# Performance work log

Hardware: AMD Instinct MI355X
Metric: run time of the kernel (lower is better)

## Reference

```python
import jax, jax.numpy as jnp
import numpy as np

ROPE_THETA = 10000.0


def apply_rope(q, k, cos, sin):
    # q,k: [B,H,S,D]; cos,sin: [S,D/2] -> broadcast [1,1,S,D/2]
    def rot(t):
        t2 = t.reshape(*t.shape[:-1], -1, 2)  # [B,H,S,D/2,2]
        te, to = t2[..., 0], t2[..., 1]
        c = cos[None, None, :, :]
        s = sin[None, None, :, :]
        re = te * c - to * s
        im = te * s + to * c
        return jnp.stack([re, im], axis=-1).reshape(t.shape)
    return rot(q), rot(k)


def setup_inputs() -> dict:
    key = jax.random.key(0)
    ks = jax.random.split(key, 4)
    B, S, D, H = 2, 2048, 1024, 16
    hd = D // H
    x = jax.random.normal(ks[0], (B, S, D), dtype=jnp.float32)
    # causal boolean mask (True = keep)
    mask = jnp.tril(jnp.ones((S, S), dtype=bool))[None, None]
    # rotary tables
    inv_freq = 1.0 / (ROPE_THETA ** (jnp.arange(0, hd, 2, dtype=jnp.float32) / hd))  # [hd/2]
    t = jnp.arange(S, dtype=jnp.float32)
    ang = t[:, None] * inv_freq[None, :]  # [S, hd/2]
    freqs_cos = jnp.cos(ang)
    freqs_sin = jnp.sin(ang)
    W_qkv = jax.random.normal(ks[1], (D, 3 * D), dtype=jnp.float32) * 0.02
    b_qkv = jnp.zeros((3 * D,), dtype=jnp.float32)
    W_o = jax.random.normal(ks[2], (D, D), dtype=jnp.float32) * 0.02
    b_o = jnp.zeros((D,), dtype=jnp.float32)
    return {"x": x, "mask": mask, "freqs_cos": freqs_cos, "freqs_sin": freqs_sin,
            "W_qkv": W_qkv, "b_qkv": b_qkv, "W_o": W_o, "b_o": b_o}


def reference(x, mask, freqs_cos, freqs_sin, W_qkv, b_qkv, W_o, b_o):
    B, S, D = x.shape
    H = 16
    hd = D // H
    scale = hd ** -0.5
    qkv = x @ W_qkv + b_qkv  # [B,S,3D]
    q, k, v = jnp.split(qkv, 3, axis=-1)
    q = q.reshape(B, S, H, hd).transpose(0, 2, 1, 3)  # [B,H,S,hd]
    k = k.reshape(B, S, H, hd).transpose(0, 2, 1, 3)
    v = v.reshape(B, S, H, hd).transpose(0, 2, 1, 3)
    q, k = apply_rope(q, k, freqs_cos, freqs_sin)
    scores = jnp.einsum('bhqd,bhkd->bhqk', q, k) * scale
    scores = jnp.where(mask, scores, jnp.finfo(scores.dtype).min)
    attn = jax.nn.softmax(scores, axis=-1)
    out = jnp.einsum('bhqk,bhkd->bhqd', attn, v)
    out = out.transpose(0, 2, 1, 3).reshape(B, S, D)
    return out @ W_o + b_o
```

## Files before the change

kernel.cpp:

```cpp
#include <hip/hip_runtime.h>
#include <hip/hip_bf16.h>
#include <stdint.h>

typedef unsigned short u16;
typedef __attribute__((ext_vector_type(8))) __bf16 bf16x8;
typedef __attribute__((ext_vector_type(4))) float f32x4;
typedef __attribute__((ext_vector_type(16))) float f32x16;
typedef __attribute__((ext_vector_type(8))) u16 u16x8;

__device__ __forceinline__ u16 f2bf(float f) {
  union { float f; unsigned int u; } v; v.f = f;
  unsigned int r = v.u + 0x7fffu + ((v.u >> 16) & 1u);
  return (u16)(r >> 16);
}
__device__ __forceinline__ unsigned pack2(float lo, float hi) {
  return (unsigned)f2bf(lo) | ((unsigned)f2bf(hi) << 16);
}

__device__ __forceinline__ f32x4 mfma16(bf16x8 a, bf16x8 b, f32x4 c) {
  return __builtin_amdgcn_mfma_f32_16x16x32_bf16(a, b, c, 0, 0, 0);
}
__device__ __forceinline__ f32x16 mfma32(bf16x8 a, bf16x8 b, f32x16 c) {
  return __builtin_amdgcn_mfma_f32_32x32x16_bf16(a, b, c, 0, 0, 0);
}

__device__ __forceinline__ void gload16(const void* g, void* l) {
  __builtin_amdgcn_global_load_lds((const __attribute__((address_space(1))) void*)g,
                                   (__attribute__((address_space(3))) void*)l,
                                   16, 0, 0);
}

__global__ void cast_bf16_kernel(const float* __restrict__ in, u16* __restrict__ out, int n) {
  int i = (blockIdx.x * 256 + threadIdx.x) * 8;
  if (i >= n) return;
  const float4* p = (const float4*)(in + i);
  float4 a = p[0], b = p[1];
  u16x8 o;
  o[0] = f2bf(a.x); o[1] = f2bf(a.y); o[2] = f2bf(a.z); o[3] = f2bf(a.w);
  o[4] = f2bf(b.x); o[5] = f2bf(b.y); o[6] = f2bf(b.z); o[7] = f2bf(b.w);
  *(u16x8*)(out + i) = o;
}

__global__ void transpose_cast_k(const float* __restrict__ in, u16* __restrict__ out,
                                 int R, int Ccols) {
  __shared__ float tile[64][65];
  const int c0 = (int)blockIdx.x << 6, r0 = (int)blockIdx.y << 6;
  const int tx = threadIdx.x & 63, ty = threadIdx.x >> 6;
#pragma unroll
  for (int i = ty; i < 64; i += 4)
    tile[i][tx] = in[(size_t)(r0 + i) * Ccols + c0 + tx];
  __syncthreads();
#pragma unroll
  for (int i = ty; i < 64; i += 4)
    out[(size_t)(c0 + i) * R + r0 + tx] = f2bf(tile[tx][i]);
}

__global__ __launch_bounds__(256, 2)
void gemm_qkv(const u16* __restrict__ A, const u16* __restrict__ Bt,
              const float* __restrict__ bias,
              const float* __restrict__ fc, const float* __restrict__ fs,
              u16* __restrict__ qr, u16* __restrict__ kr, u16* __restrict__ vr) {
  const int K = 1024;
  __shared__ __align__(16) u16 smem[128 * 136];
  u16* const As = smem;
  u16* const Bs = smem + 128 * 32;
  const int m0 = (int)(blockIdx.x / 24) << 7;
  const int n0 = (int)(blockIdx.x % 24) << 7;
  const int tid = threadIdx.x;
  const int l = tid & 63, lg = l >> 4, ll = l & 15;
  const int w = tid >> 6;
  const int wr = (w >> 1) << 6, wc = (w & 1) << 6;
  const int srow = tid >> 2, scol = (tid & 3) << 3;
  const u16* ga = A + (size_t)(m0 + srow) * K + scol;
  const u16* gb = Bt + (size_t)(n0 + srow) * K + scol;
  u16* la0 = &As[srow * 32 + scol];
  u16* la1 = &As[(srow + 64) * 32 + scol];
  u16* lb0 = &Bs[srow * 32 + scol];
  u16* lb1 = &Bs[(srow + 64) * 32 + scol];
  const size_t K64 = (size_t)64 * K;
  f32x4 acc[4][4] = {};
  for (int kt = 0; kt < K; kt += 32) {
    gload16(ga + kt, la0);
    gload16(ga + kt + K64, la1);
    gload16(gb + kt, lb0);
    gload16(gb + kt + K64, lb1);
    __syncthreads();
    bf16x8 a[4], b[4];
#pragma unroll
    for (int i = 0; i < 4; ++i) {
      a[i] = *(const bf16x8*)&As[(wr + i * 16 + ll) * 32 + lg * 8];
      b[i] = *(const bf16x8*)&Bs[(wc + i * 16 + ll) * 32 + lg * 8];
    }
#pragma unroll
    for (int mi = 0; mi < 4; ++mi)
#pragma unroll
      for (int ni = 0; ni < 4; ++ni)
        acc[mi][ni] = mfma16(a[mi], b[ni], acc[mi][ni]);
    __syncthreads();
  }
  const int sec = n0 >> 10;
  u16* const dst = (sec == 0) ? qr : (sec == 1) ? kr : vr;
  const int h0 = (n0 & 1023) >> 6;
#pragma unroll
  for (int ni = 0; ni < 4; ++ni) {
    const int cc = wc + ni * 16 + ll;
    const int n = n0 + cc;
    const int d = n & 63;
    const float bi_ = bias[n];
    const int i2 = d >> 1;
    const bool odd = d & 1;
#pragma unroll
    for (int mi = 0; mi < 4; ++mi) {
#pragma unroll
      for (int r = 0; r < 4; ++r) {
        const int rr = wr + mi * 16 + lg * 4 + r;
        const int s = (m0 + rr) & 2047;
        float v = acc[mi][ni][r] + bi_;
        if (sec < 2) {
          const float c = fc[s * 32 + i2], sn = fs[s * 32 + i2];
          const float p = __shfl_xor(v, 1);
          v = odd ? (p * sn + v * c) : (v * c - p * sn);
          if (sec == 0) v *= 0.125f;
        }
        smem[rr * 136 + cc] = f2bf(v);
      }
    }
  }
  __syncthreads();
#pragma unroll
  for (int it = 0; it < 8; ++it) {
    const int c = it * 256 + tid;
    const int j = c & 7, hh = (c >> 3) & 1, rr = c >> 4;
    const int row = m0 + rr;
    const int bb = row >> 11, ss = row & 2047;
    const uint4 val = *(const uint4*)&smem[rr * 136 + hh * 64 + j * 8];
    *(uint4*)&dst[((size_t)(((bb << 4) + h0 + hh) << 11) + ss) * 64 + j * 8] = val;
  }
}

__global__ __launch_bounds__(256, 2)
void gemm_bt(const u16* __restrict__ A, const u16* __restrict__ Bt,
             const float* __restrict__ bias, float* __restrict__ C,
             int M, int N, int K) {
  __shared__ u16 As[128 * 32];
  __shared__ u16 Bs[128 * 32];
  const int nb = N >> 7;
  const int m0 = (int)(blockIdx.x / nb) << 7;
  const int n0 = (int)(blockIdx.x % nb) << 7;
  const int tid = threadIdx.x;
  const int l = tid & 63, lg = l >> 4, ll = l & 15;
  const int w = tid >> 6;
  const int wr = (w >> 1) << 6, wc = (w & 1) << 6;
  const int srow = tid >> 2, scol = (tid & 3) << 3;
  const u16* ga = A + (size_t)(m0 + srow) * K + scol;
  const u16* gb = Bt + (size_t)(n0 + srow) * K + scol;
  u16* la0 = &As[srow * 32 + scol];
  u16* la1 = &As[(srow + 64) * 32 + scol];
  u16* lb0 = &Bs[srow * 32 + scol];
  u16* lb1 = &Bs[(srow + 64) * 32 + scol];
  const size_t K64 = (size_t)64 * K;
  f32x4 acc[4][4] = {};
  for (int kt = 0; kt < K; kt += 32) {
    gload16(ga + kt, la0);
    gload16(ga + kt + K64, la1);
    gload16(gb + kt, lb0);
    gload16(gb + kt + K64, lb1);
    __syncthreads();
    bf16x8 a[4], b[4];
#pragma unroll
    for (int i = 0; i < 4; ++i) {
      a[i] = *(const bf16x8*)&As[(wr + i * 16 + ll) * 32 + lg * 8];
      b[i] = *(const bf16x8*)&Bs[(wc + i * 16 + ll) * 32 + lg * 8];
    }
#pragma unroll
    for (int mi = 0; mi < 4; ++mi)
#pragma unroll
      for (int ni = 0; ni < 4; ++ni)
        acc[mi][ni] = mfma16(a[mi], b[ni], acc[mi][ni]);
    __syncthreads();
  }
#pragma unroll
  for (int mi = 0; mi < 4; ++mi) {
#pragma unroll
    for (int r = 0; r < 4; ++r) {
      const int row = m0 + wr + mi * 16 + lg * 4 + r;
      float* crow = C + (size_t)row * N + n0 + wc;
#pragma unroll
      for (int ni = 0; ni < 4; ++ni)
        crow[ni * 16 + ll] = acc[mi][ni][r] + bias[n0 + wc + ni * 16 + ll];
    }
  }
}

__global__ void v_transpose_bf16(const u16* __restrict__ vr, u16* __restrict__ vt) {
  __shared__ u16 tile[64][66];
  const int bh = blockIdx.x;
  const int s0 = (int)blockIdx.y << 6;
  const int tx = threadIdx.x & 63, ty = threadIdx.x >> 6;
#pragma unroll
  for (int i = ty; i < 64; i += 4)
    tile[i][tx] = vr[((size_t)bh * 2048 + s0 + i) * 64 + tx];
  __syncthreads();
#pragma unroll
  for (int i = ty; i < 64; i += 4)
    vt[((size_t)bh * 64 + i) * 2048 + s0 + tx] = tile[tx][i];
}

__global__ __launch_bounds__(256, 2)
void attn_k(const u16* __restrict__ qr, const u16* __restrict__ kr,
            const u16* __restrict__ vt, u16* __restrict__ aout) {
  __shared__ __align__(16) char kvlds[16384];
  const int bi = (int)blockIdx.x;
  const int bh = bi & 31;
  const int qt = (bi < 256) ? (15 - (bi >> 5)) : ((bi - 256) >> 5);
  const int tid = threadIdx.x;
  const int w = tid >> 6, l = tid & 63, hi = l >> 5, ql = l & 31;
  const u16* Q  = qr + (size_t)bh * (2048 * 64);
  const u16* Kp = kr + (size_t)bh * (2048 * 64);
  const u16* Vp = vt + (size_t)bh * (64 * 2048);
  const int q0w = (qt << 7) + (w << 5);
  const int qg = q0w + ql;
  bf16x8 qf[4];
#pragma unroll
  for (int mi = 0; mi < 4; ++mi)
    qf[mi] = *(const bf16x8*)&Q[(size_t)qg * 64 + mi * 16 + hi * 8];
  const int sr = tid >> 2, sc = (tid & 3) * 32;
  const int wo0 = (sr * 128 + sc) ^ ((sr & 7) << 4);
  const int wo1 = (sr * 128 + sc + 16) ^ ((sr & 7) << 4);
  const char* kga = (const char*)(Kp + (size_t)sr * 64) + sc;
  const char* vga = (const char*)(Vp + (size_t)sr * 2048) + sc;
  const int swz = (ql & 7) << 4;
  f32x16 oa = {}, ob = {};
  float mrow = -1e30f, lp = 0.f;
  const int nch = 2 * qt + 2;
  uint4 sk0 = *(const uint4*)(kga), sk1 = *(const uint4*)(kga + 16);
  uint4 sv0 = *(const uint4*)(vga), sv1 = *(const uint4*)(vga + 16);
  for (int ch = 0; ch < nch; ++ch) {
    asm volatile("s_waitcnt vmcnt(0)" ::: "memory");
    asm volatile("s_barrier" ::: "memory");
    *(uint4*)(kvlds + wo0) = sk0;
    *(uint4*)(kvlds + wo1) = sk1;
    *(uint4*)(kvlds + 8192 + wo0) = sv0;
    *(uint4*)(kvlds + 8192 + wo1) = sv1;
    if (ch + 1 < nch) {
      const size_t kof = (size_t)(ch + 1) * 8192;
      const size_t vof = (size_t)(ch + 1) * 128;
      sk0 = *(const uint4*)(kga + kof); sk1 = *(const uint4*)(kga + kof + 16);
      sv0 = *(const uint4*)(vga + vof); sv1 = *(const uint4*)(vga + vof + 16);
    }
    asm volatile("s_waitcnt lgkmcnt(0)" ::: "memory");
    asm volatile("s_barrier" ::: "memory");
    const int kb = ch << 6;
    if (kb > q0w + 31) continue;
    f32x16 s0 = {}, s1 = {};
#pragma unroll
    for (int mi = 0; mi < 4; ++mi) {
      const int cb = mi * 32 + hi * 16;
      const bf16x8 k0 = *(const bf16x8*)(kvlds + ((ql * 128 + cb) ^ swz));
      const bf16x8 k1 = *(const bf16x8*)(kvlds + (((32 + ql) * 128 + cb) ^ swz));
      s0 = mfma32(k0, qf[mi], s0);
      s1 = mfma32(k1, qf[mi], s1);
    }
    if (kb + 63 > q0w) {
#pragma unroll
      for (int r = 0; r < 16; ++r) {
        const int kvo = (r & 3) + 8 * (r >> 2) + 4 * hi;
        if (kb + kvo > qg) s0[r] = -1e30f;
        if (kb + 32 + kvo > qg) s1[r] = -1e30f;
      }
    }
    float mx = s0[0];
#pragma unroll
    for (int r = 1; r < 16; ++r) mx = fmaxf(mx, s0[r]);
#pragma unroll
    for (int r = 0; r < 16; ++r) mx = fmaxf(mx, s1[r]);
    mx = fmaxf(mx, __shfl_xor(mx, 32));
    if (!__all(mx <= mrow + 8.f)) {
      const float mn = fmaxf(mrow, mx);
      const float esc = __expf(mrow - mn);
      mrow = mn;
      lp *= esc;
#pragma unroll
      for (int r = 0; r < 16; ++r) { oa[r] *= esc; ob[r] *= esc; }
    }
    float p0[16], p1[16];
#pragma unroll
    for (int r = 0; r < 16; ++r) {
      p0[r] = __expf(s0[r] - mrow);
      p1[r] = __expf(s1[r] - mrow);
      lp += p0[r] + p1[r];
    }
    bf16x8 pb[4];
#pragma unroll
    for (int s = 0; s < 2; ++s) {
      const float* ps = s ? p1 : p0;
#pragma unroll
      for (int j = 0; j < 2; ++j) {
        const unsigned X0 = pack2(ps[j * 8 + 0], ps[j * 8 + 1]);
        const unsigned X1 = pack2(ps[j * 8 + 2], ps[j * 8 + 3]);
        const unsigned Y0 = pack2(ps[j * 8 + 4], ps[j * 8 + 5]);
        const unsigned Y1 = pack2(ps[j * 8 + 6], ps[j * 8 + 7]);
        const unsigned sX0 = (unsigned)__shfl_xor((int)X0, 32);
        const unsigned sX1 = (unsigned)__shfl_xor((int)X1, 32);
        const unsigned sY0 = (unsigned)__shfl_xor((int)Y0, 32);
        const unsigned sY1 = (unsigned)__shfl_xor((int)Y1, 32);
        union { unsigned u[4]; bf16x8 v; } t;
        t.u[0] = hi ? sY0 : X0;
        t.u[1] = hi ? sY1 : X1;
        t.u[2] = hi ? Y0 : sX0;
        t.u[3] = hi ? Y1 : sX1;
        pb[s * 2 + j] = t.v;
      }
    }
#pragma unroll
    for (int jj = 0; jj < 4; ++jj) {
      const int cb = jj * 32 + hi * 16;
      const bf16x8 va = *(const bf16x8*)(kvlds + 8192 + ((ql * 128 + cb) ^ swz));
      const bf16x8 vb = *(const bf16x8*)(kvlds + 8192 + (((32 + ql) * 128 + cb) ^ swz));
      oa = mfma32(va, pb[jj], oa);
      ob = mfma32(vb, pb[jj], ob);
    }
  }
  lp += __shfl_xor(lp, 32);
  const float inv = 1.0f / lp;
  const int hcol = (bh & 15) << 6;
  const int tok = ((bh >> 4) << 11) + qg;
  unsigned* orow = (unsigned*)(aout + (size_t)tok * 1024 + hcol);
#pragma unroll
  for (int r = 0; r < 16; r += 2) {
    const int d0 = (r & 3) + 8 * (r >> 2) + 4 * hi;
    orow[d0 >> 1]        = pack2(oa[r] * inv, oa[r + 1] * inv);
    orow[(32 + d0) >> 1] = pack2(ob[r] * inv, ob[r + 1] * inv);
  }
}

extern "C" void kernel_launch(void* const* d_in, const int* in_sizes, int n_in,
                              void* d_out, int out_size, void* d_ws, size_t ws_size,
                              hipStream_t stream) {
  const float* x    = (const float*)d_in[0];
  const float* fc   = (const float*)d_in[2];
  const float* fs   = (const float*)d_in[3];
  const float* Wqkv = (const float*)d_in[4];
  const float* bqkv = (const float*)d_in[5];
  const float* Wo   = (const float*)d_in[6];
  const float* bo   = (const float*)d_in[7];
  float* out = (float*)d_out;

  size_t off = 0;
  auto alloc = [&](size_t bytes) {
    void* p = (char*)d_ws + off;
    off += (bytes + 255) & ~(size_t)255;
    return p;
  };
  u16*   xb   = (u16*)  alloc(4096ull * 1024 * 2);
  u16*   wqt  = (u16*)  alloc(3072ull * 1024 * 2);
  u16*   wot  = (u16*)  alloc(1024ull * 1024 * 2);
  u16*   qr_  = (u16*)  alloc(32ull * 2048 * 64 * 2);
  u16*   kr_  = (u16*)  alloc(32ull * 2048 * 64 * 2);
  u16*   vr_  = (u16*)  alloc(32ull * 2048 * 64 * 2);
  u16*   vt_  = (u16*)  alloc(32ull * 64 * 2048 * 2);
  u16*   ao_  = (u16*)  alloc(4096ull * 1024 * 2);

  cast_bf16_kernel<<<2048, 256, 0, stream>>>(x, xb, 4096 * 1024);
  transpose_cast_k<<<dim3(48, 16), 256, 0, stream>>>(Wqkv, wqt, 1024, 3072);
  transpose_cast_k<<<dim3(16, 16), 256, 0, stream>>>(Wo, wot, 1024, 1024);
  gemm_qkv<<<dim3(32 * 24), 256, 0, stream>>>(xb, wqt, bqkv, fc, fs, qr_, kr_, vr_);
  v_transpose_bf16<<<dim3(32, 32), 256, 0, stream>>>(vr_, vt_);
  attn_k<<<dim3(512), 256, 0, stream>>>(qr_, kr_, vt_, ao_);
  gemm_bt<<<dim3(32 * 8), 256, 0, stream>>>(ao_, wot, bo, out, 4096, 1024, 1024);
}
```

Measured before the change: 140.5 us.

## Double GEMM K-step to 64 and store V transposed in contiguous chunks

Both GEMMs now stage 64 K-elements per barrier pair instead of 32, splitting each stage into two 32-wide LDS halves, which halves the number of loop iterations and syncs. gemm_qkv's launch bound goes to 3 blocks per CU. The V transpose writes each 64x64 tile as a contiguous 8 KB chunk, so attention loads of V become linear and use the same offset as K. The larger LDS footprint and the occupancy hint may raise register pressure or limit residency.

After: 133.4 us. -5.0%, faster.

```diff
diff --git a/kernel.cpp b/kernel.cpp
--- a/kernel.cpp
+++ b/kernel.cpp
@@ -55,7 +55,7 @@
     out[(size_t)(c0 + i) * R + r0 + tx] = f2bf(tile[tx][i]);
 }
 
-__global__ __launch_bounds__(256, 2)
+__global__ __launch_bounds__(256, 3)
 void gemm_qkv(const u16* __restrict__ A, const u16* __restrict__ Bt,
               const float* __restrict__ bias,
               const float* __restrict__ fc, const float* __restrict__ fs,
@@ -63,7 +63,7 @@
   const int K = 1024;
   __shared__ __align__(16) u16 smem[128 * 136];
   u16* const As = smem;
-  u16* const Bs = smem + 128 * 32;
+  u16* const Bs = smem + 8192;
   const int m0 = (int)(blockIdx.x / 24) << 7;
   const int n0 = (int)(blockIdx.x % 24) << 7;
   const int tid = threadIdx.x;
@@ -73,29 +73,36 @@
   const int srow = tid >> 2, scol = (tid & 3) << 3;
   const u16* ga = A + (size_t)(m0 + srow) * K + scol;
   const u16* gb = Bt + (size_t)(n0 + srow) * K + scol;
-  u16* la0 = &As[srow * 32 + scol];
-  u16* la1 = &As[(srow + 64) * 32 + scol];
-  u16* lb0 = &Bs[srow * 32 + scol];
-  u16* lb1 = &Bs[(srow + 64) * 32 + scol];
   const size_t K64 = (size_t)64 * K;
+  u16* const la00 = &As[srow * 32 + scol];
+  u16* const la01 = &As[4096 + srow * 32 + scol];
+  u16* const la10 = &As[(srow + 64) * 32 + scol];
+  u16* const la11 = &As[4096 + (srow + 64) * 32 + scol];
+  u16* const lb00 = &Bs[srow * 32 + scol];
+  u16* const lb01 = &Bs[4096 + srow * 32 + scol];
+  u16* const lb10 = &Bs[(srow + 64) * 32 + scol];
+  u16* const lb11 = &Bs[4096 + (srow + 64) * 32 + scol];
   f32x4 acc[4][4] = {};
-  for (int kt = 0; kt < K; kt += 32) {
-    gload16(ga + kt, la0);
-    gload16(ga + kt + K64, la1);
-    gload16(gb + kt, lb0);
-    gload16(gb + kt + K64, lb1);
+  for (int kt = 0; kt < K; kt += 64) {
+    gload16(ga + kt, la00);       gload16(ga + kt + 32, la01);
+    gload16(ga + kt + K64, la10); gload16(ga + kt + K64 + 32, la11);
+    gload16(gb + kt, lb00);       gload16(gb + kt + 32, lb01);
+    gload16(gb + kt + K64, lb10); gload16(gb + kt + K64 + 32, lb11);
     __syncthreads();
-    bf16x8 a[4], b[4];
-#pragma unroll
-    for (int i = 0; i < 4; ++i) {
-      a[i] = *(const bf16x8*)&As[(wr + i * 16 + ll) * 32 + lg * 8];
-      b[i] = *(const bf16x8*)&Bs[(wc + i * 16 + ll) * 32 + lg * 8];
-    }
-#pragma unroll
-    for (int mi = 0; mi < 4; ++mi)
-#pragma unroll
-      for (int ni = 0; ni < 4; ++ni)
-        acc[mi][ni] = mfma16(a[mi], b[ni], acc[mi][ni]);
+#pragma unroll
+    for (int h = 0; h < 2; ++h) {
+      bf16x8 a[4], b[4];
+#pragma unroll
+      for (int i = 0; i < 4; ++i) {
+        a[i] = *(const bf16x8*)&As[h * 4096 + (wr + i * 16 + ll) * 32 + lg * 8];
+        b[i] = *(const bf16x8*)&Bs[h * 4096 + (wc + i * 16 + ll) * 32 + lg * 8];
+      }
+#pragma unroll
+      for (int mi = 0; mi < 4; ++mi)
+#pragma unroll
+        for (int ni = 0; ni < 4; ++ni)
+          acc[mi][ni] = mfma16(a[mi], b[ni], acc[mi][ni]);
+    }
     __syncthreads();
   }
   const int sec = n0 >> 10;
@@ -142,8 +149,8 @@
 void gemm_bt(const u16* __restrict__ A, const u16* __restrict__ Bt,
              const float* __restrict__ bias, float* __restrict__ C,
              int M, int N, int K) {
-  __shared__ u16 As[128 * 32];
-  __shared__ u16 Bs[128 * 32];
+  __shared__ __align__(16) u16 As[2 * 128 * 32];
+  __shared__ __align__(16) u16 Bs[2 * 128 * 32];
   const int nb = N >> 7;
   const int m0 = (int)(blockIdx.x / nb) << 7;
   const int n0 = (int)(blockIdx.x % nb) << 7;
@@ -154,29 +161,36 @@
   const int srow = tid >> 2, scol = (tid & 3) << 3;
   const u16* ga = A + (size_t)(m0 + srow) * K + scol;
   const u16* gb = Bt + (size_t)(n0 + srow) * K + scol;
-  u16* la0 = &As[srow * 32 + scol];
-  u16* la1 = &As[(srow + 64) * 32 + scol];
-  u16* lb0 = &Bs[srow * 32 + scol];
-  u16* lb1 = &Bs[(srow + 64) * 32 + scol];
   const size_t K64 = (size_t)64 * K;
+  u16* const la00 = &As[srow * 32 + scol];
+  u16* const la01 = &As[4096 + srow * 32 + scol];
+  u16* const la10 = &As[(srow + 64) * 32 + scol];
+  u16* const la11 = &As[4096 + (srow + 64) * 32 + scol];
+  u16* const lb00 = &Bs[srow * 32 + scol];
+  u16* const lb01 = &Bs[4096 + srow * 32 + scol];
+  u16* const lb10 = &Bs[(srow + 64) * 32 + scol];
+  u16* const lb11 = &Bs[4096 + (srow + 64) * 32 + scol];
   f32x4 acc[4][4] = {};
-  for (int kt = 0; kt < K; kt += 32) {
-    gload16(ga + kt, la0);
-    gload16(ga + kt + K64, la1);
-    gload16(gb + kt, lb0);
-    gload16(gb + kt + K64, lb1);
+  for (int kt = 0; kt < K; kt += 64) {
+    gload16(ga + kt, la00);       gload16(ga + kt + 32, la01);
+    gload16(ga + kt + K64, la10); gload16(ga + kt + K64 + 32, la11);
+    gload16(gb + kt, lb00);       gload16(gb + kt + 32, lb01);
+    gload16(gb + kt + K64, lb10); gload16(gb + kt + K64 + 32, lb11);
     __syncthreads();
-    bf16x8 a[4], b[4];
-#pragma unroll
-    for (int i = 0; i < 4; ++i) {
-      a[i] = *(const bf16x8*)&As[(wr + i * 16 + ll) * 32 + lg * 8];
-      b[i] = *(const bf16x8*)&Bs[(wc + i * 16 + ll) * 32 + lg * 8];
-    }
-#pragma unroll
-    for (int mi = 0; mi < 4; ++mi)
-#pragma unroll
-      for (int ni = 0; ni < 4; ++ni)
-        acc[mi][ni] = mfma16(a[mi], b[ni], acc[mi][ni]);
+#pragma unroll
+    for (int h = 0; h < 2; ++h) {
+      bf16x8 a[4], b[4];
+#pragma unroll
+      for (int i = 0; i < 4; ++i) {
+        a[i] = *(const bf16x8*)&As[h * 4096 + (wr + i * 16 + ll) * 32 + lg * 8];
+        b[i] = *(const bf16x8*)&Bs[h * 4096 + (wc + i * 16 + ll) * 32 + lg * 8];
+      }
+#pragma unroll
+      for (int mi = 0; mi < 4; ++mi)
+#pragma unroll
+        for (int ni = 0; ni < 4; ++ni)
+          acc[mi][ni] = mfma16(a[mi], b[ni], acc[mi][ni]);
+    }
     __syncthreads();
   }
 #pragma unroll
@@ -192,7 +206,7 @@
   }
 }
 
-__global__ void v_transpose_bf16(const u16* __restrict__ vr, u16* __restrict__ vt) {
+__global__ void v_transpose_bf16(const u16* __restrict__ vr, u16* __restrict__ vtc) {
   __shared__ u16 tile[64][66];
   const int bh = blockIdx.x;
   const int s0 = (int)blockIdx.y << 6;
@@ -201,14 +215,15 @@
   for (int i = ty; i < 64; i += 4)
     tile[i][tx] = vr[((size_t)bh * 2048 + s0 + i) * 64 + tx];
   __syncthreads();
+  u16* const outc = vtc + ((size_t)bh * 32 + (s0 >> 6)) * 4096;
 #pragma unroll
   for (int i = ty; i < 64; i += 4)
-    vt[((size_t)bh * 64 + i) * 2048 + s0 + tx] = tile[tx][i];
+    outc[i * 64 + tx] = tile[tx][i];
 }
 
 __global__ __launch_bounds__(256, 2)
 void attn_k(const u16* __restrict__ qr, const u16* __restrict__ kr,
-            const u16* __restrict__ vt, u16* __restrict__ aout) {
+            const u16* __restrict__ vtc, u16* __restrict__ aout) {
   __shared__ __align__(16) char kvlds[16384];
   const int bi = (int)blockIdx.x;
   const int bh = bi & 31;
@@ -217,7 +232,6 @@
   const int w = tid >> 6, l = tid & 63, hi = l >> 5, ql = l & 31;
   const u16* Q  = qr + (size_t)bh * (2048 * 64);
   const u16* Kp = kr + (size_t)bh * (2048 * 64);
-  const u16* Vp = vt + (size_t)bh * (64 * 2048);
   const int q0w = (qt << 7) + (w << 5);
   const int qg = q0w + ql;
   bf16x8 qf[4];
@@ -228,7 +242,7 @@
   const int wo0 = (sr * 128 + sc) ^ ((sr & 7) << 4);
   const int wo1 = (sr * 128 + sc + 16) ^ ((sr & 7) << 4);
   const char* kga = (const char*)(Kp + (size_t)sr * 64) + sc;
-  const char* vga = (const char*)(Vp + (size_t)sr * 2048) + sc;
+  const char* vga = (const char*)(vtc + (size_t)bh * 32 * 4096) + sr * 128 + sc;
   const int swz = (ql & 7) << 4;
   f32x16 oa = {}, ob = {};
   float mrow = -1e30f, lp = 0.f;
@@ -244,9 +258,8 @@
     *(uint4*)(kvlds + 8192 + wo1) = sv1;
     if (ch + 1 < nch) {
       const size_t kof = (size_t)(ch + 1) * 8192;
-      const size_t vof = (size_t)(ch + 1) * 128;
       sk0 = *(const uint4*)(kga + kof); sk1 = *(const uint4*)(kga + kof + 16);
-      sv0 = *(const uint4*)(vga + vof); sv1 = *(const uint4*)(vga + vof + 16);
+      sv0 = *(const uint4*)(vga + kof); sv1 = *(const uint4*)(vga + kof + 16);
     }
     asm volatile("s_waitcnt lgkmcnt(0)" ::: "memory");
     asm volatile("s_barrier" ::: "memory");
@@ -358,14 +371,14 @@
   u16*   qr_  = (u16*)  alloc(32ull * 2048 * 64 * 2);
   u16*   kr_  = (u16*)  alloc(32ull * 2048 * 64 * 2);
   u16*   vr_  = (u16*)  alloc(32ull * 2048 * 64 * 2);
-  u16*   vt_  = (u16*)  alloc(32ull * 64 * 2048 * 2);
+  u16*   vtc_ = (u16*)  alloc(32ull * 32 * 4096 * 2);
   u16*   ao_  = (u16*)  alloc(4096ull * 1024 * 2);
 
   cast_bf16_kernel<<<2048, 256, 0, stream>>>(x, xb, 4096 * 1024);
   transpose_cast_k<<<dim3(48, 16), 256, 0, stream>>>(Wqkv, wqt, 1024, 3072);
   transpose_cast_k<<<dim3(16, 16), 256, 0, stream>>>(Wo, wot, 1024, 1024);
   gemm_qkv<<<dim3(32 * 24), 256, 0, stream>>>(xb, wqt, bqkv, fc, fs, qr_, kr_, vr_);
-  v_transpose_bf16<<<dim3(32, 32), 256, 0, stream>>>(vr_, vt_);
-  attn_k<<<dim3(512), 256, 0, stream>>>(qr_, kr_, vt_, ao_);
+  v_transpose_bf16<<<dim3(32, 32), 256, 0, stream>>>(vr_, vtc_);
+  attn_k<<<dim3(512), 256, 0, stream>>>(qr_, kr_, vtc_, ao_);
   gemm_bt<<<dim3(32 * 8), 256, 0, stream>>>(ao_, wot, bo, out, 4096, 1024, 1024);
 }
```
